# Kernel optimization log

Hardware: AMD Instinct MI355X
Metric: run time of the kernel (lower is better)

The kernel has to match this reference:

```python
import jax, jax.numpy as jnp
import numpy as np

D_MODEL = 1024
D_FF = 4096
N_HEADS = 16
D_K = D_MODEL // N_HEADS
EPS = 1e-6
NEG_INF = 1.0e9


def _layer_norm(x, g, b):
    mu = jnp.mean(x, axis=-1, keepdims=True)
    var = jnp.mean(jnp.square(x - mu), axis=-1, keepdims=True)
    return (x - mu) / jnp.sqrt(var + EPS) * g + b


def setup_inputs() -> dict:
    key = jax.random.key(0)
    ks = jax.random.split(key, 16)
    s = 1.0 / np.sqrt(D_MODEL)
    inp = {
        'x': jax.random.normal(ks[0], (4, 2048, D_MODEL), dtype=jnp.float32),
        'e_mask': jnp.ones((4, 1, 2048), dtype=jnp.int32),
        'ln1_g': jnp.ones((D_MODEL,), jnp.float32),
        'ln1_b': jnp.zeros((D_MODEL,), jnp.float32),
        'wq': jax.random.normal(ks[1], (D_MODEL, D_MODEL), jnp.float32) * s,
        'bq': jnp.zeros((D_MODEL,), jnp.float32),
        'wk': jax.random.normal(ks[2], (D_MODEL, D_MODEL), jnp.float32) * s,
        'bk': jnp.zeros((D_MODEL,), jnp.float32),
        'wv': jax.random.normal(ks[3], (D_MODEL, D_MODEL), jnp.float32) * s,
        'bv': jnp.zeros((D_MODEL,), jnp.float32),
        'w0': jax.random.normal(ks[4], (D_MODEL, D_MODEL), jnp.float32) * s,
        'b0': jnp.zeros((D_MODEL,), jnp.float32),
        'ln2_g': jnp.ones((D_MODEL,), jnp.float32),
        'ln2_b': jnp.zeros((D_MODEL,), jnp.float32),
        'w1': jax.random.normal(ks[5], (D_MODEL, D_FF), jnp.float32) * s,
        'b1': jnp.zeros((D_FF,), jnp.float32),
        'w2': jax.random.normal(ks[6], (D_FF, D_MODEL), jnp.float32) * (1.0 / np.sqrt(D_FF)),
        'b2': jnp.zeros((D_MODEL,), jnp.float32),
    }
    return inp


def reference(x, e_mask, ln1_g, ln1_b, wq, bq, wk, bk, wv, bv, w0, b0,
              ln2_g, ln2_b, w1, b1, w2, b2):
    B, S, _ = x.shape
    # --- pre-LN multihead attention (dropout = identity in eval) ---
    x1 = _layer_norm(x, ln1_g, ln1_b)
    q = (x1 @ wq + bq).reshape(B, S, N_HEADS, D_K).transpose(0, 2, 1, 3)
    k = (x1 @ wk + bk).reshape(B, S, N_HEADS, D_K).transpose(0, 2, 1, 3)
    v = (x1 @ wv + bv).reshape(B, S, N_HEADS, D_K).transpose(0, 2, 1, 3)
    scores = jnp.einsum('bhqd,bhkd->bhqk', q, k) / np.sqrt(D_K).astype(np.float32)
    mask = e_mask[:, None, :, :]  # [B,1,1,S] broadcast over heads and queries
    scores = jnp.where(mask == 0, -NEG_INF, scores)
    attn = jax.nn.softmax(scores, axis=-1)
    ctx = jnp.einsum('bhqk,bhkd->bhqd', attn, v)
    ctx = ctx.transpose(0, 2, 1, 3).reshape(B, S, D_MODEL)
    x = x + (ctx @ w0 + b0)
    # --- pre-LN feed-forward ---
    x2 = _layer_norm(x, ln2_g, ln2_b)
    h = jax.nn.relu(x2 @ w1 + b1)
    x = x + (h @ w2 + b2)
    return x
```

## Files before the change

### kernel.cpp

```cpp
#include <hip/hip_runtime.h>
#include <cstdint>
#include <cstddef>

typedef __bf16 bf16;
typedef __bf16 bf16x8 __attribute__((ext_vector_type(8)));
typedef __bf16 bf16x4 __attribute__((ext_vector_type(4)));
typedef float  f32x4  __attribute__((ext_vector_type(4)));
typedef float  f32x16 __attribute__((ext_vector_type(16)));

#define D_MODEL 1024
#define D_FF    4096
#define SEQ     2048
#define NB      4
#define NH      16
#define DKH     64
#define MTOT    (NB * SEQ)

__device__ __forceinline__ void gl_lds16(const void* g, void* l) {
  __builtin_amdgcn_global_load_lds(
      (__attribute__((address_space(1))) unsigned int*)(void*)g,
      (__attribute__((address_space(3))) unsigned int*)l, 16, 0, 0);
}

__device__ __forceinline__ unsigned cvtpk(float lo, float hi_) {
  unsigned r;
  asm("v_cvt_pk_bf16_f32 %0, %1, %2" : "=v"(r) : "v"(lo), "v"(hi_));
  return r;
}
__device__ __forceinline__ void pl32swap(unsigned& a, unsigned& b) {
  asm volatile("v_permlane32_swap_b32 %0, %1" : "+v"(a), "+v"(b));
}

__global__ __launch_bounds__(256) void k_transp(const float* __restrict__ W,
                                                bf16* __restrict__ Wt, int R, int C) {
  __shared__ float tile[32][33];
  const int c0 = blockIdx.x * 32, r0 = blockIdx.y * 32;
  const int t = threadIdx.x;
  const int rl = t >> 5, cl = t & 31;
#pragma unroll
  for (int i = 0; i < 4; ++i)
    tile[rl + i * 8][cl] = W[(size_t)(r0 + rl + i * 8) * C + c0 + cl];
  __syncthreads();
#pragma unroll
  for (int i = 0; i < 4; ++i)
    Wt[(size_t)(c0 + rl + i * 8) * R + r0 + cl] = (bf16)tile[cl][rl + i * 8];
}

__global__ __launch_bounds__(256) void k_ln(const float* __restrict__ x,
                                            const float* __restrict__ g,
                                            const float* __restrict__ b,
                                            bf16* __restrict__ out) {
  const int row = blockIdx.x;
  const int t = threadIdx.x;
  const float4 v = ((const float4*)(x + (size_t)row * D_MODEL))[t];
  float s  = v.x + v.y + v.z + v.w;
  float s2 = v.x * v.x + v.y * v.y + v.z * v.z + v.w * v.w;
#pragma unroll
  for (int off = 1; off < 64; off <<= 1) {
    s  += __shfl_xor(s, off);
    s2 += __shfl_xor(s2, off);
  }
  __shared__ float red[8];
  const int wv = t >> 6;
  if ((t & 63) == 0) { red[wv] = s; red[4 + wv] = s2; }
  __syncthreads();
  s  = red[0] + red[1] + red[2] + red[3];
  s2 = red[4] + red[5] + red[6] + red[7];
  const float mu   = s * (1.f / D_MODEL);
  const float var  = s2 * (1.f / D_MODEL) - mu * mu;
  const float rstd = rsqrtf(var + 1e-6f);
  const float4 gv = ((const float4*)g)[t];
  const float4 bv = ((const float4*)b)[t];
  bf16x4 o;
  o[0] = (bf16)((v.x - mu) * rstd * gv.x + bv.x);
  o[1] = (bf16)((v.y - mu) * rstd * gv.y + bv.y);
  o[2] = (bf16)((v.z - mu) * rstd * gv.z + bv.z);
  o[3] = (bf16)((v.w - mu) * rstd * gv.w + bv.w);
  *(bf16x4*)(out + (size_t)row * D_MODEL + t * 4) = o;
}

template <int EPI>
__global__ __launch_bounds__(512, 2) void k_gemm(
    const bf16* __restrict__ A, const bf16* __restrict__ Bt,
    const float* __restrict__ bias, const float* __restrict__ biasK,
    const float* __restrict__ biasV, float alpha,
    bf16* __restrict__ obf, float* __restrict__ of32,
    const float* __restrict__ resid,
    int M, int N, int K) {
  __shared__ char lds[2][49152];
  const int t = threadIdx.x, lane = t & 63, w = t >> 6;
  const int wm = w >> 1, wn = w & 1;

  const int gx = gridDim.x;
  const int nwg = gx * gridDim.y;
  int id = blockIdx.x + blockIdx.y * gx;
  id = (id & 7) * (nwg >> 3) + (id >> 3);
  const int tn = (id % gx) * 128;
  const int tm = (id / gx) * 256;

  const int srow = w * 16 + (lane >> 3);
  const int scol = 8 * ((lane & 7) ^ (lane >> 3));
  const bf16* aS = A  + (size_t)(tm + srow) * K + scol;
  const bf16* bS = Bt + (size_t)(tn + srow) * K + scol;
  const int dstOff = w * 2048;

  const int rA = (wm * 64 + (lane & 15)) * 128;
  const int rB = 32768 + (wn * 64 + (lane & 15)) * 128;
  const int cS0 = (((lane >> 4) * 16)      ) ^ ((lane & 7) << 4);
  const int cS1 = (64 + ((lane >> 4) * 16) ) ^ ((lane & 7) << 4);

  f32x4 acc[4][4] = {};
  const int KT = K >> 6;

  gl_lds16(aS,                 lds[0] + dstOff);
  gl_lds16(aS + 8 * K,         lds[0] + dstOff + 1024);
  gl_lds16(aS + 128 * K,       lds[0] + 16384 + dstOff);
  gl_lds16(aS + 136 * K,       lds[0] + 16384 + dstOff + 1024);
  gl_lds16(bS,                 lds[0] + 32768 + dstOff);
  gl_lds16(bS + 8 * K,         lds[0] + 32768 + dstOff + 1024);
  gl_lds16(aS + 64,            lds[1] + dstOff);
  gl_lds16(aS + 8 * K + 64,    lds[1] + dstOff + 1024);
  asm volatile("s_waitcnt vmcnt(2)" ::: "memory");
  __builtin_amdgcn_s_barrier();
  __builtin_amdgcn_sched_barrier(0);

#define RD(buf, off) (*(const bf16x8*)((buf) + (off)))
#define MM(m, n, s) acc[m][n] = __builtin_amdgcn_mfma_f32_16x16x32_bf16(a[m][s], b[n][s], acc[m][n], 0, 0, 0)

  for (int tt = 0; tt < KT; ++tt) {
    char* bufc = lds[tt & 1];
    char* bufn = lds[(tt & 1) ^ 1];
    const int k1 = (tt + 1 < KT ? tt + 1 : KT - 1) * 64;
    const int k2 = (tt + 2 < KT ? tt + 2 : KT - 1) * 64;
    bf16x8 a[4][2], b[4][2];
    a[0][0] = RD(bufc, rA + cS0);          a[0][1] = RD(bufc, rA + cS1);
    a[1][0] = RD(bufc, rA + 2048 + cS0);   a[1][1] = RD(bufc, rA + 2048 + cS1);
    b[0][0] = RD(bufc, rB + cS0);
    b[1][0] = RD(bufc, rB + 2048 + cS0);
    b[2][0] = RD(bufc, rB + 4096 + cS0);
    b[3][0] = RD(bufc, rB + 6144 + cS0);
    gl_lds16(aS + 128 * K + k1, bufn + 16384 + dstOff);
    gl_lds16(aS + 136 * K + k1, bufn + 16384 + dstOff + 1024);
    __builtin_amdgcn_s_setprio(1);
    MM(0,0,0); MM(0,1,0); MM(0,2,0); MM(0,3,0);
    MM(1,0,0); MM(1,1,0); MM(1,2,0); MM(1,3,0);
    __builtin_amdgcn_s_setprio(0);
    a[2][0] = RD(bufc, rA + 4096 + cS0);   a[2][1] = RD(bufc, rA + 4096 + cS1);
    a[3][0] = RD(bufc, rA + 6144 + cS0);   a[3][1] = RD(bufc, rA + 6144 + cS1);
    b[0][1] = RD(bufc, rB + cS1);
    b[1][1] = RD(bufc, rB + 2048 + cS1);
    b[2][1] = RD(bufc, rB + 4096 + cS1);
    b[3][1] = RD(bufc, rB + 6144 + cS1);
    gl_lds16(bS + k1,         bufn + 32768 + dstOff);
    gl_lds16(bS + 8 * K + k1, bufn + 32768 + dstOff + 1024);
    __builtin_amdgcn_s_setprio(1);
    MM(2,0,0); MM(2,1,0); MM(2,2,0); MM(2,3,0);
    MM(3,0,0); MM(3,1,0); MM(3,2,0); MM(3,3,0);
    __builtin_amdgcn_s_setprio(0);
    asm volatile("s_waitcnt lgkmcnt(0)" ::: "memory");
    __builtin_amdgcn_s_barrier();
    __builtin_amdgcn_sched_barrier(0);
    gl_lds16(aS + k2,         bufc + dstOff);
    gl_lds16(aS + 8 * K + k2, bufc + dstOff + 1024);
    __builtin_amdgcn_s_setprio(1);
    MM(0,0,1); MM(0,1,1); MM(0,2,1); MM(0,3,1);
    MM(1,0,1); MM(1,1,1); MM(1,2,1); MM(1,3,1);
    __builtin_amdgcn_s_setprio(0);
    __builtin_amdgcn_s_setprio(1);
    MM(2,0,1); MM(2,1,1); MM(2,2,1); MM(2,3,1);
    MM(3,0,1); MM(3,1,1); MM(3,2,1); MM(3,3,1);
    __builtin_amdgcn_s_setprio(0);
    asm volatile("s_waitcnt vmcnt(2)" ::: "memory");
    __builtin_amdgcn_s_barrier();
    __builtin_amdgcn_sched_barrier(0);
  }
#undef RD
#undef MM
  asm volatile("s_waitcnt vmcnt(0)" ::: "memory");

  const int row0 = tm + wm * 64 + (lane >> 4) * 4;
  const int col0 = tn + wn * 64 + (lane & 15);
  const int which = tn >> 10;
  const float* bp = (EPI == 1) ? (which == 0 ? bias : (which == 1 ? biasK : biasV)) : bias;
  const float af_ = (EPI == 1) ? (which == 0 ? alpha : 1.f) : alpha;
  bf16* qkvB = (EPI == 1) ? obf + (size_t)which * MTOT * D_MODEL : obf;
#pragma unroll
  for (int n = 0; n < 4; ++n) {
    const int col = col0 + n * 16;
    const float bv = (EPI == 1) ? bp[col & 1023] : bp[col];
#pragma unroll
    for (int m = 0; m < 4; ++m) {
#pragma unroll
      for (int r = 0; r < 4; ++r) {
        const int row = row0 + m * 16 + r;
        float val = acc[m][n][r] + bv;
        if constexpr (EPI == 1) {
          const int bb = row >> 11, ss = row & 2047, hh = (col >> 6) & 15, dd = col & 63;
          qkvB[(((size_t)bb * NH + hh) * SEQ + ss) * DKH + dd] = (bf16)(val * af_);
        } else if constexpr (EPI == 2) {
          const size_t idx = (size_t)row * N + col;
          of32[idx] = resid[idx] + val;
        } else {
          obf[(size_t)row * N + col] = (bf16)fmaxf(val, 0.f);
        }
      }
    }
  }
}

__global__ __launch_bounds__(512, 4) void k_attn(
    const bf16* __restrict__ q, const bf16* __restrict__ k, const bf16* __restrict__ v,
    const int* __restrict__ emask, bf16* __restrict__ ctx) {
  __shared__ bf16 Kl[64 * 64];
  __shared__ bf16 Vt[64 * 64];
  __shared__ float Msk[64];
  __shared__ int MskFlag;
  const int t = threadIdx.x, lane = t & 63, w = t >> 6;
  const int hi = lane >> 5;
  const int l31 = lane & 31;
  const unsigned swz = (lane & 7) << 4;
  const int bh = blockIdx.x, b = bh >> 4, h = bh & 15;
  const int q0 = blockIdx.y * 256;
  const bf16* qp = q + (size_t)bh * SEQ * DKH;
  const bf16* kp = k + (size_t)bh * SEQ * DKH;
  const bf16* vp = v + (size_t)bh * SEQ * DKH;
  const int* mp = emask + b * SEQ;

  const int qrow = q0 + w * 32 + l31;
  const bf16* qpr = qp + (size_t)qrow * DKH + hi * 8;
  bf16x8 qf[4];
#pragma unroll
  for (int ks = 0; ks < 4; ++ks) qf[ks] = *(const bf16x8*)(qpr + ks * 16);

  const int krow = w * 8 + (lane >> 3);
  const int kcolE = (((lane & 7) * 16) ^ ((lane >> 3) << 4)) >> 1;
  const bf16* kSrc = kp + (size_t)krow * DKH + kcolE;
  char* kDst = (char*)Kl + w * 1024;

  const ushort* vU = (const ushort*)vp;
  bf16* vDst = (bf16*)((char*)Vt + (lane << 7) + ((w * 16) ^ ((lane & 7) << 4)));

  f32x16 O0 = {}, O1 = {};
  float mrun = -3e38f, lrun = 0.f;

  for (int kt = 0; kt < SEQ; kt += 64) {
    __syncthreads();
    gl_lds16(kSrc + (size_t)kt * DKH, kDst);
    union { ushort u[8]; bf16x8 v8; } vb;
#pragma unroll
    for (int j = 0; j < 8; ++j)
      vb.u[j] = vU[(size_t)(kt + w * 8 + j) * 64 + lane];
    *(bf16x8*)vDst = vb.v8;
    if (t < 64) {
      const float mv = (mp[kt + t] == 0) ? -1e9f : 0.f;
      Msk[t] = mv;
      const unsigned long long bal = __ballot(mv != 0.f);
      if (t == 0) MskFlag = (bal != 0ull);
    }
    __syncthreads();

    f32x16 s0 = {}, s1 = {};
#pragma unroll
    for (int ks = 0; ks < 4; ++ks) {
      const bf16x8 kf = *(const bf16x8*)((const char*)Kl + (l31 << 7) + ((ks * 32 + hi * 16) ^ swz));
      s0 = __builtin_amdgcn_mfma_f32_32x32x16_bf16(kf, qf[ks], s0, 0, 0, 0);
    }
#pragma unroll
    for (int ks = 0; ks < 4; ++ks) {
      const bf16x8 kf = *(const bf16x8*)((const char*)Kl + ((32 + l31) << 7) + ((ks * 32 + hi * 16) ^ swz));
      s1 = __builtin_amdgcn_mfma_f32_32x32x16_bf16(kf, qf[ks], s1, 0, 0, 0);
    }
    if (MskFlag) {
#pragma unroll
      for (int g = 0; g < 4; ++g)
#pragma unroll
        for (int j = 0; j < 4; ++j) {
          s0[g * 4 + j] += Msk[g * 8 + hi * 4 + j];
          s1[g * 4 + j] += Msk[32 + g * 8 + hi * 4 + j];
        }
    }

    float mx = s0[0];
#pragma unroll
    for (int r = 1; r < 16; ++r) mx = fmaxf(mx, s0[r]);
#pragma unroll
    for (int r = 0; r < 16; ++r) mx = fmaxf(mx, s1[r]);
    mx = fmaxf(mx, __shfl_xor(mx, 32));
    if (!__all((int)(mx - mrun <= 8.f))) {
      const float mnew = fmaxf(mrun, mx);
      const float scal = exp2f(mrun - mnew);
      mrun = mnew;
      lrun *= scal;
#pragma unroll
      for (int r = 0; r < 16; ++r) { O0[r] *= scal; O1[r] *= scal; }
    }
    float ts = 0.f;
#pragma unroll
    for (int r = 0; r < 16; ++r) { const float p = exp2f(s0[r] - mrun); s0[r] = p; ts += p; }
#pragma unroll
    for (int r = 0; r < 16; ++r) { const float p = exp2f(s1[r] - mrun); s1[r] = p; ts += p; }
    ts += __shfl_xor(ts, 32);
    lrun += ts;

#define PVSTEP(S, bsel, ks)                                                          \
    {                                                                                \
      unsigned c0 = cvtpk(S[8 * bsel + 0], S[8 * bsel + 1]);                         \
      unsigned c1 = cvtpk(S[8 * bsel + 2], S[8 * bsel + 3]);                         \
      unsigned c2 = cvtpk(S[8 * bsel + 4], S[8 * bsel + 5]);                         \
      unsigned c3 = cvtpk(S[8 * bsel + 6], S[8 * bsel + 7]);                         \
      pl32swap(c0, c2);                                                              \
      pl32swap(c1, c3);                                                              \
      union { unsigned u[4]; bf16x8 vv_; } pu = {{c0, c1, c2, c3}};                  \
      const bf16x8 vf0 = *(const bf16x8*)((const char*)Vt + (l31 << 7) + (((ks) * 32 + hi * 16) ^ swz)); \
      O0 = __builtin_amdgcn_mfma_f32_32x32x16_bf16(vf0, pu.vv_, O0, 0, 0, 0);        \
      const bf16x8 vf1 = *(const bf16x8*)((const char*)Vt + ((32 + l31) << 7) + (((ks) * 32 + hi * 16) ^ swz)); \
      O1 = __builtin_amdgcn_mfma_f32_32x32x16_bf16(vf1, pu.vv_, O1, 0, 0, 0);        \
    }
    PVSTEP(s0, 0, 0)
    PVSTEP(s0, 1, 1)
    PVSTEP(s1, 0, 2)
    PVSTEP(s1, 1, 3)
#undef PVSTEP
  }

  const float rl = 1.f / lrun;
  bf16* cp = ctx + ((size_t)b * SEQ + qrow) * D_MODEL + h * 64;
#pragma unroll
  for (int r = 0; r < 16; ++r) {
    const int d0 = (r & 3) + 8 * (r >> 2) + hi * 4;
    cp[d0]      = (bf16)(O0[r] * rl);
    cp[32 + d0] = (bf16)(O1[r] * rl);
  }
}

extern "C" void kernel_launch(void* const* d_in, const int* in_sizes, int n_in,
                              void* d_out, int out_size, void* d_ws, size_t ws_size,
                              hipStream_t stream) {
  (void)in_sizes; (void)n_in; (void)out_size; (void)ws_size;
  const float* x    = (const float*)d_in[0];
  const int*   em   = (const int*)d_in[1];
  const float* ln1g = (const float*)d_in[2];
  const float* ln1b = (const float*)d_in[3];
  const float* wq   = (const float*)d_in[4];
  const float* bq   = (const float*)d_in[5];
  const float* wk   = (const float*)d_in[6];
  const float* bk   = (const float*)d_in[7];
  const float* wv   = (const float*)d_in[8];
  const float* bv   = (const float*)d_in[9];
  const float* w0   = (const float*)d_in[10];
  const float* b0   = (const float*)d_in[11];
  const float* ln2g = (const float*)d_in[12];
  const float* ln2b = (const float*)d_in[13];
  const float* w1   = (const float*)d_in[14];
  const float* b1   = (const float*)d_in[15];
  const float* w2   = (const float*)d_in[16];
  const float* b2   = (const float*)d_in[17];
  float* out = (float*)d_out;

  char* ws = (char*)d_ws;
  const size_t MB = 1u << 20;
  bf16* wqT = (bf16*)(ws + 0 * MB);
  bf16* w0T = (bf16*)(ws + 6 * MB);
  bf16* w1T = (bf16*)(ws + 8 * MB);
  bf16* w2T = (bf16*)(ws + 16 * MB);
  bf16* x1  = (bf16*)(ws + 24 * MB);
  bf16* qB  = (bf16*)(ws + 40 * MB);
  bf16* kB  = (bf16*)(ws + 56 * MB);
  bf16* vB  = (bf16*)(ws + 72 * MB);
  bf16* cB  = (bf16*)(ws + 88 * MB);
  bf16* hB  = (bf16*)(ws + 40 * MB);

  k_transp<<<dim3(32, 32),  256, 0, stream>>>(wq, wqT,                   1024, 1024);
  k_transp<<<dim3(32, 32),  256, 0, stream>>>(wk, wqT + 1024 * 1024,     1024, 1024);
  k_transp<<<dim3(32, 32),  256, 0, stream>>>(wv, wqT + 2 * 1024 * 1024, 1024, 1024);
  k_transp<<<dim3(32, 32),  256, 0, stream>>>(w0, w0T, 1024, 1024);
  k_transp<<<dim3(128, 32), 256, 0, stream>>>(w1, w1T, 1024, 4096);
  k_transp<<<dim3(32, 128), 256, 0, stream>>>(w2, w2T, 4096, 1024);

  k_ln<<<MTOT, 256, 0, stream>>>(x, ln1g, ln1b, x1);

  k_gemm<1><<<dim3(24, MTOT / 256), 512, 0, stream>>>(
      x1, wqT, bq, bk, bv, 0.125f * 1.44269504f, qB, nullptr, nullptr, MTOT, 3072, 1024);

  k_attn<<<dim3(64, 8), 512, 0, stream>>>(qB, kB, vB, em, cB);

  const dim3 g1024(8, MTOT / 256);
  k_gemm<2><<<g1024, 512, 0, stream>>>(cB, w0T, b0, nullptr, nullptr, 1.0f, nullptr, out, x, MTOT, 1024, 1024);

  k_ln<<<MTOT, 256, 0, stream>>>(out, ln2g, ln2b, x1);

  k_gemm<3><<<dim3(32, MTOT / 256), 512, 0, stream>>>(x1, w1T, b1, nullptr, nullptr, 1.0f, hB, nullptr, nullptr, MTOT, 4096, 1024);

  k_gemm<2><<<g1024, 512, 0, stream>>>(hB, w2T, b2, nullptr, nullptr, 1.0f, nullptr, out, out, MTOT, 1024, 4096);
}
```

Before: 545.7 us.

## Enlarge GEMM tiles to 256x256 and halve attention block size

The GEMM output tile per workgroup doubles from 256x128 to 256x256. Each of the 8 waves now computes a 128x64 sub-tile with 128 accumulator registers, which raises operand reuse per LDS read and per global load. The cost is 128KB of LDS per block, which leaves room for only one resident block per CU, and the N=1024 GEMMs now launch just 128 workgroups. The attention kernel is reshaped to 256 threads handling 128 queries per block, with each wave staging twice as much K/V. Its running-max reduction is rewritten as a tree of three-input maxes.

```diff
diff --git a/kernel.cpp b/kernel.cpp
--- a/kernel.cpp
+++ b/kernel.cpp
@@ -29,6 +29,9 @@
 }
 __device__ __forceinline__ void pl32swap(unsigned& a, unsigned& b) {
   asm volatile("v_permlane32_swap_b32 %0, %1" : "+v"(a), "+v"(b));
+}
+__device__ __forceinline__ float max3f(float a, float b, float c) {
+  return fmaxf(fmaxf(a, b), c);
 }
 
 __global__ __launch_bounds__(256) void k_transp(const float* __restrict__ W,
@@ -87,98 +90,130 @@
     bf16* __restrict__ obf, float* __restrict__ of32,
     const float* __restrict__ resid,
     int M, int N, int K) {
-  __shared__ char lds[2][49152];
+  __shared__ char lds[2][65536];
   const int t = threadIdx.x, lane = t & 63, w = t >> 6;
-  const int wm = w >> 1, wn = w & 1;
+  const int wm = w >> 2, wn = w & 3;
 
   const int gx = gridDim.x;
   const int nwg = gx * gridDim.y;
   int id = blockIdx.x + blockIdx.y * gx;
   id = (id & 7) * (nwg >> 3) + (id >> 3);
-  const int tn = (id % gx) * 128;
+  const int tn = (id % gx) * 256;
   const int tm = (id / gx) * 256;
 
-  const int srow = w * 16 + (lane >> 3);
   const int scol = 8 * ((lane & 7) ^ (lane >> 3));
-  const bf16* aS = A  + (size_t)(tm + srow) * K + scol;
-  const bf16* bS = Bt + (size_t)(tn + srow) * K + scol;
-  const int dstOff = w * 2048;
-
-  const int rA = (wm * 64 + (lane & 15)) * 128;
+  const bf16* aS[4];
+  const bf16* bS[4];
+#pragma unroll
+  for (int i = 0; i < 4; ++i) {
+    aS[i] = A  + (size_t)(tm + 8 * (w + 8 * i) + (lane >> 3)) * K + scol;
+    bS[i] = Bt + (size_t)(tn + 8 * (w + 8 * i) + (lane >> 3)) * K + scol;
+  }
+  const int dA = w * 1024;
+  const int dB = 32768 + w * 1024;
+
+  const int rA = (wm * 128 + (lane & 15)) * 128;
   const int rB = 32768 + (wn * 64 + (lane & 15)) * 128;
-  const int cS0 = (((lane >> 4) * 16)      ) ^ ((lane & 7) << 4);
-  const int cS1 = (64 + ((lane >> 4) * 16) ) ^ ((lane & 7) << 4);
-
-  f32x4 acc[4][4] = {};
+  const int cS0 = (((lane >> 4) * 16)     ) ^ ((lane & 7) << 4);
+  const int cS1 = (64 + ((lane >> 4) * 16)) ^ ((lane & 7) << 4);
+
+  f32x4 acc[8][4] = {};
   const int KT = K >> 6;
 
-  gl_lds16(aS,                 lds[0] + dstOff);
-  gl_lds16(aS + 8 * K,         lds[0] + dstOff + 1024);
-  gl_lds16(aS + 128 * K,       lds[0] + 16384 + dstOff);
-  gl_lds16(aS + 136 * K,       lds[0] + 16384 + dstOff + 1024);
-  gl_lds16(bS,                 lds[0] + 32768 + dstOff);
-  gl_lds16(bS + 8 * K,         lds[0] + 32768 + dstOff + 1024);
-  gl_lds16(aS + 64,            lds[1] + dstOff);
-  gl_lds16(aS + 8 * K + 64,    lds[1] + dstOff + 1024);
+#pragma unroll
+  for (int i = 0; i < 4; ++i) {
+    gl_lds16(aS[i], lds[0] + dA + i * 8192);
+    gl_lds16(bS[i], lds[0] + dB + i * 8192);
+  }
+  gl_lds16(aS[0] + 64, lds[1] + dA);
+  gl_lds16(aS[1] + 64, lds[1] + dA + 8192);
   asm volatile("s_waitcnt vmcnt(2)" ::: "memory");
   __builtin_amdgcn_s_barrier();
   __builtin_amdgcn_sched_barrier(0);
 
 #define RD(buf, off) (*(const bf16x8*)((buf) + (off)))
-#define MM(m, n, s) acc[m][n] = __builtin_amdgcn_mfma_f32_16x16x32_bf16(a[m][s], b[n][s], acc[m][n], 0, 0, 0)
 
   for (int tt = 0; tt < KT; ++tt) {
     char* bufc = lds[tt & 1];
     char* bufn = lds[(tt & 1) ^ 1];
     const int k1 = (tt + 1 < KT ? tt + 1 : KT - 1) * 64;
     const int k2 = (tt + 2 < KT ? tt + 2 : KT - 1) * 64;
-    bf16x8 a[4][2], b[4][2];
-    a[0][0] = RD(bufc, rA + cS0);          a[0][1] = RD(bufc, rA + cS1);
-    a[1][0] = RD(bufc, rA + 2048 + cS0);   a[1][1] = RD(bufc, rA + 2048 + cS1);
-    b[0][0] = RD(bufc, rB + cS0);
-    b[1][0] = RD(bufc, rB + 2048 + cS0);
-    b[2][0] = RD(bufc, rB + 4096 + cS0);
-    b[3][0] = RD(bufc, rB + 6144 + cS0);
-    gl_lds16(aS + 128 * K + k1, bufn + 16384 + dstOff);
-    gl_lds16(aS + 136 * K + k1, bufn + 16384 + dstOff + 1024);
+    bf16x8 a0[4][2], a1[4][2], b[4][2];
+#pragma unroll
+    for (int m = 0; m < 4; ++m) {
+      a0[m][0] = RD(bufc, rA + m * 2048 + cS0);
+      a0[m][1] = RD(bufc, rA + m * 2048 + cS1);
+    }
+#pragma unroll
+    for (int n = 0; n < 2; ++n) {
+      b[n][0] = RD(bufc, rB + n * 2048 + cS0);
+      b[n][1] = RD(bufc, rB + n * 2048 + cS1);
+    }
+    gl_lds16(aS[2] + k1, bufn + dA + 2 * 8192);
+    gl_lds16(aS[3] + k1, bufn + dA + 3 * 8192);
+    gl_lds16(bS[0] + k1, bufn + dB);
     __builtin_amdgcn_s_setprio(1);
-    MM(0,0,0); MM(0,1,0); MM(0,2,0); MM(0,3,0);
-    MM(1,0,0); MM(1,1,0); MM(1,2,0); MM(1,3,0);
+#pragma unroll
+    for (int m = 0; m < 4; ++m)
+#pragma unroll
+      for (int n = 0; n < 2; ++n)
+#pragma unroll
+        for (int s = 0; s < 2; ++s)
+          acc[m][n] = __builtin_amdgcn_mfma_f32_16x16x32_bf16(a0[m][s], b[n][s], acc[m][n], 0, 0, 0);
     __builtin_amdgcn_s_setprio(0);
-    a[2][0] = RD(bufc, rA + 4096 + cS0);   a[2][1] = RD(bufc, rA + 4096 + cS1);
-    a[3][0] = RD(bufc, rA + 6144 + cS0);   a[3][1] = RD(bufc, rA + 6144 + cS1);
-    b[0][1] = RD(bufc, rB + cS1);
-    b[1][1] = RD(bufc, rB + 2048 + cS1);
-    b[2][1] = RD(bufc, rB + 4096 + cS1);
-    b[3][1] = RD(bufc, rB + 6144 + cS1);
-    gl_lds16(bS + k1,         bufn + 32768 + dstOff);
-    gl_lds16(bS + 8 * K + k1, bufn + 32768 + dstOff + 1024);
+#pragma unroll
+    for (int n = 2; n < 4; ++n) {
+      b[n][0] = RD(bufc, rB + n * 2048 + cS0);
+      b[n][1] = RD(bufc, rB + n * 2048 + cS1);
+    }
+#pragma unroll
+    for (int m = 0; m < 4; ++m) {
+      a1[m][0] = RD(bufc, rA + (4 + m) * 2048 + cS0);
+      a1[m][1] = RD(bufc, rA + (4 + m) * 2048 + cS1);
+    }
+    gl_lds16(bS[1] + k1, bufn + dB + 8192);
+    gl_lds16(bS[2] + k1, bufn + dB + 2 * 8192);
+    gl_lds16(bS[3] + k1, bufn + dB + 3 * 8192);
     __builtin_amdgcn_s_setprio(1);
-    MM(2,0,0); MM(2,1,0); MM(2,2,0); MM(2,3,0);
-    MM(3,0,0); MM(3,1,0); MM(3,2,0); MM(3,3,0);
+#pragma unroll
+    for (int m = 0; m < 4; ++m)
+#pragma unroll
+      for (int n = 2; n < 4; ++n)
+#pragma unroll
+        for (int s = 0; s < 2; ++s)
+          acc[m][n] = __builtin_amdgcn_mfma_f32_16x16x32_bf16(a0[m][s], b[n][s], acc[m][n], 0, 0, 0);
     __builtin_amdgcn_s_setprio(0);
     asm volatile("s_waitcnt lgkmcnt(0)" ::: "memory");
     __builtin_amdgcn_s_barrier();
     __builtin_amdgcn_sched_barrier(0);
-    gl_lds16(aS + k2,         bufc + dstOff);
-    gl_lds16(aS + 8 * K + k2, bufc + dstOff + 1024);
+    gl_lds16(aS[0] + k2, bufc + dA);
+    gl_lds16(aS[1] + k2, bufc + dA + 8192);
     __builtin_amdgcn_s_setprio(1);
-    MM(0,0,1); MM(0,1,1); MM(0,2,1); MM(0,3,1);
-    MM(1,0,1); MM(1,1,1); MM(1,2,1); MM(1,3,1);
+#pragma unroll
+    for (int m = 0; m < 4; ++m)
+#pragma unroll
+      for (int n = 0; n < 2; ++n)
+#pragma unroll
+        for (int s = 0; s < 2; ++s)
+          acc[4 + m][n] = __builtin_amdgcn_mfma_f32_16x16x32_bf16(a1[m][s], b[n][s], acc[4 + m][n], 0, 0, 0);
     __builtin_amdgcn_s_setprio(0);
     __builtin_amdgcn_s_setprio(1);
-    MM(2,0,1); MM(2,1,1); MM(2,2,1); MM(2,3,1);
-    MM(3,0,1); MM(3,1,1); MM(3,2,1); MM(3,3,1);
+#pragma unroll
+    for (int m = 0; m < 4; ++m)
+#pragma unroll
+      for (int n = 2; n < 4; ++n)
+#pragma unroll
+        for (int s = 0; s < 2; ++s)
+          acc[4 + m][n] = __builtin_amdgcn_mfma_f32_16x16x32_bf16(a1[m][s], b[n][s], acc[4 + m][n], 0, 0, 0);
     __builtin_amdgcn_s_setprio(0);
     asm volatile("s_waitcnt vmcnt(2)" ::: "memory");
     __builtin_amdgcn_s_barrier();
     __builtin_amdgcn_sched_barrier(0);
   }
 #undef RD
-#undef MM
   asm volatile("s_waitcnt vmcnt(0)" ::: "memory");
 
-  const int row0 = tm + wm * 64 + (lane >> 4) * 4;
+  const int row0 = tm + wm * 128 + (lane >> 4) * 4;
   const int col0 = tn + wn * 64 + (lane & 15);
   const int which = tn >> 10;
   const float* bp = (EPI == 1) ? (which == 0 ? bias : (which == 1 ? biasK : biasV)) : bias;
@@ -189,7 +224,7 @@
     const int col = col0 + n * 16;
     const float bv = (EPI == 1) ? bp[col & 1023] : bp[col];
 #pragma unroll
-    for (int m = 0; m < 4; ++m) {
+    for (int m = 0; m < 8; ++m) {
 #pragma unroll
       for (int r = 0; r < 4; ++r) {
         const int row = row0 + m * 16 + r;
@@ -208,7 +243,7 @@
   }
 }
 
-__global__ __launch_bounds__(512, 4) void k_attn(
+__global__ __launch_bounds__(256, 4) void k_attn(
     const bf16* __restrict__ q, const bf16* __restrict__ k, const bf16* __restrict__ v,
     const int* __restrict__ emask, bf16* __restrict__ ctx) {
   __shared__ bf16 Kl[64 * 64];
@@ -220,7 +255,7 @@
   const int l31 = lane & 31;
   const unsigned swz = (lane & 7) << 4;
   const int bh = blockIdx.x, b = bh >> 4, h = bh & 15;
-  const int q0 = blockIdx.y * 256;
+  const int q0 = blockIdx.y * 128;
   const bf16* qp = q + (size_t)bh * SEQ * DKH;
   const bf16* kp = k + (size_t)bh * SEQ * DKH;
   const bf16* vp = v + (size_t)bh * SEQ * DKH;
@@ -232,25 +267,31 @@
 #pragma unroll
   for (int ks = 0; ks < 4; ++ks) qf[ks] = *(const bf16x8*)(qpr + ks * 16);
 
-  const int krow = w * 8 + (lane >> 3);
   const int kcolE = (((lane & 7) * 16) ^ ((lane >> 3) << 4)) >> 1;
-  const bf16* kSrc = kp + (size_t)krow * DKH + kcolE;
-  char* kDst = (char*)Kl + w * 1024;
+  const bf16* kSrc0 = kp + (size_t)(w * 16 + (lane >> 3)) * DKH + kcolE;
+  const bf16* kSrc1 = kSrc0 + (size_t)8 * DKH;
+  char* kDst0 = (char*)Kl + w * 2048;
+  char* kDst1 = kDst0 + 1024;
 
   const ushort* vU = (const ushort*)vp;
-  bf16* vDst = (bf16*)((char*)Vt + (lane << 7) + ((w * 16) ^ ((lane & 7) << 4)));
+  bf16* vDst0 = (bf16*)((char*)Vt + (lane << 7) + ((w * 32)      ^ ((lane & 7) << 4)));
+  bf16* vDst1 = (bf16*)((char*)Vt + (lane << 7) + ((w * 32 + 16) ^ ((lane & 7) << 4)));
 
   f32x16 O0 = {}, O1 = {};
   float mrun = -3e38f, lrun = 0.f;
 
   for (int kt = 0; kt < SEQ; kt += 64) {
     __syncthreads();
-    gl_lds16(kSrc + (size_t)kt * DKH, kDst);
-    union { ushort u[8]; bf16x8 v8; } vb;
-#pragma unroll
-    for (int j = 0; j < 8; ++j)
-      vb.u[j] = vU[(size_t)(kt + w * 8 + j) * 64 + lane];
-    *(bf16x8*)vDst = vb.v8;
+    gl_lds16(kSrc0 + (size_t)kt * DKH, kDst0);
+    gl_lds16(kSrc1 + (size_t)kt * DKH, kDst1);
+    union { ushort u[8]; bf16x8 v8; } vb0, vb1;
+#pragma unroll
+    for (int j = 0; j < 8; ++j) {
+      vb0.u[j] = vU[(size_t)(kt + w * 16 + j) * 64 + lane];
+      vb1.u[j] = vU[(size_t)(kt + w * 16 + 8 + j) * 64 + lane];
+    }
+    *(bf16x8*)vDst0 = vb0.v8;
+    *(bf16x8*)vDst1 = vb1.v8;
     if (t < 64) {
       const float mv = (mp[kt + t] == 0) ? -1e9f : 0.f;
       Msk[t] = mv;
@@ -280,11 +321,15 @@
         }
     }
 
-    float mx = s0[0];
-#pragma unroll
-    for (int r = 1; r < 16; ++r) mx = fmaxf(mx, s0[r]);
-#pragma unroll
-    for (int r = 0; r < 16; ++r) mx = fmaxf(mx, s1[r]);
+    const float m00 = max3f(s0[0], s0[1], s0[2]),  m01 = max3f(s0[3], s0[4], s0[5]);
+    const float m02 = max3f(s0[6], s0[7], s0[8]),  m03 = max3f(s0[9], s0[10], s0[11]);
+    const float m04 = max3f(s0[12], s0[13], s0[14]), m05 = max3f(s0[15], s1[0], s1[1]);
+    const float m06 = max3f(s1[2], s1[3], s1[4]),  m07 = max3f(s1[5], s1[6], s1[7]);
+    const float m08 = max3f(s1[8], s1[9], s1[10]), m09 = max3f(s1[11], s1[12], s1[13]);
+    const float m10 = fmaxf(s1[14], s1[15]);
+    const float n0 = max3f(m00, m01, m02), n1 = max3f(m03, m04, m05);
+    const float n2 = max3f(m06, m07, m08), n3 = fmaxf(m09, m10);
+    float mx = fmaxf(max3f(n0, n1, n2), n3);
     mx = fmaxf(mx, __shfl_xor(mx, 32));
     if (!__all((int)(mx - mrun <= 8.f))) {
       const float mnew = fmaxf(mrun, mx);
@@ -379,17 +424,17 @@
 
   k_ln<<<MTOT, 256, 0, stream>>>(x, ln1g, ln1b, x1);
 
-  k_gemm<1><<<dim3(24, MTOT / 256), 512, 0, stream>>>(
+  k_gemm<1><<<dim3(12, MTOT / 256), 512, 0, stream>>>(
       x1, wqT, bq, bk, bv, 0.125f * 1.44269504f, qB, nullptr, nullptr, MTOT, 3072, 1024);
 
-  k_attn<<<dim3(64, 8), 512, 0, stream>>>(qB, kB, vB, em, cB);
-
-  const dim3 g1024(8, MTOT / 256);
+  k_attn<<<dim3(64, 16), 256, 0, stream>>>(qB, kB, vB, em, cB);
+
+  const dim3 g1024(4, MTOT / 256);
   k_gemm<2><<<g1024, 512, 0, stream>>>(cB, w0T, b0, nullptr, nullptr, 1.0f, nullptr, out, x, MTOT, 1024, 1024);
 
   k_ln<<<MTOT, 256, 0, stream>>>(out, ln2g, ln2b, x1);
 
-  k_gemm<3><<<dim3(32, MTOT / 256), 512, 0, stream>>>(x1, w1T, b1, nullptr, nullptr, 1.0f, hB, nullptr, nullptr, MTOT, 4096, 1024);
+  k_gemm<3><<<dim3(16, MTOT / 256), 512, 0, stream>>>(x1, w1T, b1, nullptr, nullptr, 1.0f, hB, nullptr, nullptr, MTOT, 4096, 1024);
 
   k_gemm<2><<<g1024, 512, 0, stream>>>(hB, w2T, b2, nullptr, nullptr, 1.0f, nullptr, out, out, MTOT, 1024, 4096);
 }
```

Result: slower. 569.7 us (+4.4%).
